# Optimization experiments

Hardware: AMD Instinct MI355X
Metric: run time of the kernel (lower is better)

The kernel has to match this reference:

```python
import jax, jax.numpy as jnp
import numpy as np

HEADS = 8
CHANNELS = 256
RR = 1
DH = CHANNELS // RR                 # per-head channels
ATT = HEADS * DH                    # 2048
# exact scale from the torch module
SCALE = (1.0 / np.sqrt(CHANNELS // RR)) / np.sqrt(2.0 / (CHANNELS + 3 * ATT)) * np.sqrt(2.0 / (CHANNELS + ATT))


def setup_inputs() -> dict:
    key = jax.random.key(0)
    k1, k2, k3, k4, k5 = jax.random.split(key, 5)
    x = jax.random.normal(k1, (8, CHANNELS, 32, 32), dtype=jnp.float32)
    # 1x1 conv weights stored as [out_ch, in_ch]
    w_in = jax.random.normal(k2, (3 * ATT, CHANNELS), dtype=jnp.float32) * (1.0 / np.sqrt(CHANNELS))
    b_in = jax.random.normal(k3, (3 * ATT,), dtype=jnp.float32) * 0.02
    w_out = jax.random.normal(k4, (CHANNELS, ATT), dtype=jnp.float32) * (1.0 / np.sqrt(ATT))
    b_out = jax.random.normal(k5, (CHANNELS,), dtype=jnp.float32) * 0.02
    return {"x": x, "w_in": w_in, "b_in": b_in, "w_out": w_out, "b_out": b_out}


def reference(x, w_in, b_in, w_out, b_out):
    n, c, h, w = x.shape
    L = h * w
    xf = x.reshape(n, c, L)
    # 1x1 conv in = channel-mixing matmul, then fixed scale
    scaled = (jnp.einsum('ncl,oc->nol', xf, w_in) + b_in[:, None]) * jnp.float32(SCALE)
    s = scaled.reshape(n, HEADS, 3 * DH, L)
    q, k, v = s[:, :, :DH], s[:, :, DH:2 * DH], s[:, :, 2 * DH:]   # each (n, H, DH, L)
    att = jnp.einsum('nhdl,nhdm->nhlm', q, k)                       # (n, H, L, L)
    # softmax over the FLATTENED L*L axis (global per head), as in the torch code
    att = jax.nn.softmax(att.reshape(n, HEADS, L * L), axis=2).reshape(n, HEADS, L, L)
    out = jnp.einsum('nhdl,nhlm->nhdm', v, att)                     # (n, H, DH, L)
    out = out.reshape(n, ATT, L)
    out = jnp.einsum('nal,ca->ncl', out, w_out) + b_out[:, None]
    return out.reshape(n, c, h, w)
```

## Files before the change

### kernel.cpp

```cpp
#include <hip/hip_runtime.h>
#include <hip/hip_bf16.h>


typedef __bf16 bf16x8 __attribute__((ext_vector_type(8)));
typedef __bf16 bf16x4 __attribute__((ext_vector_type(4)));
typedef float f32x4 __attribute__((ext_vector_type(4)));
typedef float f32x16 __attribute__((ext_vector_type(16)));
typedef __hip_bfloat16 bf16;

__device__ __forceinline__ void async_copy16(const void* g, void* s) {
    __builtin_amdgcn_global_load_lds(
        (const __attribute__((address_space(1))) unsigned int*)g,
        (__attribute__((address_space(3))) unsigned int*)s, 16, 0, 0);
}

__device__ __forceinline__ bf16x8 scale8(bf16x8 v, float s) {
    bf16x8 r;
#pragma unroll
    for (int e = 0; e < 8; ++e) r[e] = (__bf16)((float)v[e] * s);
    return r;
}

__global__ __launch_bounds__(256)
void gemm_nt(const bf16* __restrict__ A, const bf16* __restrict__ B, void* __restrict__ Cvoid,
             int M, int N, int K, int lda, int ldb, int ldc,
             long asn, long ash, long bsn, long bsh, long csn, long csh,
             int H, int mode, const float* __restrict__ bias, const float* __restrict__ Zp,
             float scale,
             bf16* __restrict__ outQ, bf16* __restrict__ outK, bf16* __restrict__ outV)
{
    __shared__ __align__(16) bf16 smem[17408];
    bf16* Alds = smem;
    bf16* Blds = smem + 8192;

    const int tid  = threadIdx.x;
    const int wave = tid >> 6;
    const int lane = tid & 63;
    const int z  = blockIdx.z;
    const int zn = z / H, zh = z % H;

    const bf16* Ab = A + zn * asn + zh * ash;
    const bf16* Bb = B + zn * bsn + zh * bsh;

    const long tM = (long)blockIdx.y * 128;
    const long tN = (long)blockIdx.x * 128;

    const int wr   = (wave >> 1) * 64;
    const int wc   = (wave & 1) * 64;
    const int l15  = lane & 15;
    const int quad = lane >> 4;

    f32x4 acc[4][4] = {};

    const int kiters = K >> 6;
    const bool regB = (mode == 4);

#pragma unroll
    for (int i = 0; i < 4; ++i) {
        const int flat = i * 256 + tid;
        const int row  = flat >> 3;
        const int kcs  = (flat & 7) ^ (row & 7);
        async_copy16(Ab + (tM + row) * (long)lda + kcs * 8,
                     (char*)Alds + (long)(i * 256 + wave * 64) * 16);
        if (!regB) {
            async_copy16(Bb + (tN + row) * (long)ldb + kcs * 8,
                         (char*)Blds + (long)(i * 256 + wave * 64) * 16);
        }
    }
    if (regB) {
        const float zi0 = 1.0f / Zp[zn * 8 + zh * 4];
#pragma unroll
        for (int i = 0; i < 4; ++i) {
            const int flat = i * 256 + tid;
            const int row  = flat >> 3;
            const int kcs  = (flat & 7) ^ (row & 7);
            bf16x8 b = *(const bf16x8*)(Bb + (tN + row) * (long)ldb + kcs * 8);
            *(bf16x8*)((char*)Blds + (long)flat * 16) = scale8(b, zi0);
        }
    }

    bf16x8 pfA[4], pfB[4];
    for (int kt = 0; kt < kiters; ++kt) {
        __syncthreads();
        const bool has_next = (kt + 1 < kiters);
        float zin = 1.0f;
        if (has_next) {
            const long kof = (long)(kt + 1) * 64;
            if (regB) zin = 1.0f / Zp[zn * 8 + zh * 4 + ((kt + 1) >> 2)];
#pragma unroll
            for (int i = 0; i < 4; ++i) {
                const int flat = i * 256 + tid;
                const int row  = flat >> 3;
                const int kcs  = (flat & 7) ^ (row & 7);
                pfA[i] = *(const bf16x8*)(Ab + (tM + row) * (long)lda + kof + kcs * 8);
                pfB[i] = *(const bf16x8*)(Bb + (tN + row) * (long)ldb + kof + kcs * 8);
            }
        }
#pragma unroll
        for (int kk = 0; kk < 2; ++kk) {
            bf16x8 af[4], bfv[4];
#pragma unroll
            for (int i = 0; i < 4; ++i) {
                const int r = wr + i * 16 + l15;
                af[i] = *(const bf16x8*)(Alds + r * 64 + ((kk * 4 + quad) ^ (r & 7)) * 8);
            }
#pragma unroll
            for (int j = 0; j < 4; ++j) {
                const int r = wc + j * 16 + l15;
                bfv[j] = *(const bf16x8*)(Blds + r * 64 + ((kk * 4 + quad) ^ (r & 7)) * 8);
            }
#pragma unroll
            for (int i = 0; i < 4; ++i)
#pragma unroll
                for (int j = 0; j < 4; ++j)
                    acc[i][j] = __builtin_amdgcn_mfma_f32_16x16x32_bf16(af[i], bfv[j], acc[i][j], 0, 0, 0);
        }
        if (has_next) {
            __builtin_amdgcn_sched_barrier(0);
            __builtin_amdgcn_s_barrier();
            __builtin_amdgcn_sched_barrier(0);
#pragma unroll
            for (int i = 0; i < 4; ++i) {
                const int flat = i * 256 + tid;
                *(bf16x8*)((char*)Alds + (long)flat * 16) = pfA[i];
                *(bf16x8*)((char*)Blds + (long)flat * 16) = regB ? scale8(pfB[i], zin) : pfB[i];
            }
        }
    }

    if (mode >= 3) {
        float* C = (float*)Cvoid + zn * csn + zh * csh;
#pragma unroll
        for (int i = 0; i < 4; ++i)
#pragma unroll
            for (int j = 0; j < 4; ++j)
#pragma unroll
                for (int r = 0; r < 4; ++r) {
                    const long row = tM + wr + i * 16 + quad * 4 + r;
                    const long col = tN + wc + j * 16 + l15;
                    if (mode == 4) {
                        const float v = acc[i][j][r] + (zh == 0 ? bias[row] : 0.0f);
                        atomicAdd(&C[row * (long)ldc + col], v);
                    } else {
                        C[row * (long)ldc + col] = acc[i][j][r] + bias[row];
                    }
                }
        return;
    }

    const int x    = blockIdx.x;
    const int part = x % 6;
    const int nh   = zn * 8 + x / 6;
    const int d0   = (part & 1) * 128;
    const int by   = blockIdx.y;

    __syncthreads();
    if (part < 4) {
#pragma unroll
        for (int i = 0; i < 4; ++i)
#pragma unroll
            for (int j = 0; j < 4; ++j)
#pragma unroll
                for (int r = 0; r < 4; ++r) {
                    const int row = wr + i * 16 + quad * 4 + r;
                    const int col = wc + j * 16 + l15;
                    const float v = (acc[i][j][r] + bias[tN + col]) * scale;
                    const int c32 = col >> 3;
                    const int slot = (c32 & 8) | ((c32 & 7) ^ (row & 7));
                    smem[row * 128 + slot * 8 + (col & 7)] = __float2bfloat16(v);
                }
        __syncthreads();
        bf16* dst = (part < 2) ? outQ : outK;
#pragma unroll
        for (int k = 0; k < 8; ++k) {
            const int flat = k * 256 + tid;
            const int seg  = flat >> 6, ln = flat & 63;
            const int lb   = seg >> 3, wloc = seg & 7;
            const int row  = lb * 32 + (ln & 31);
            const int c32  = wloc * 2 + (ln >> 5);
            const int slot = (c32 & 8) | ((c32 & 7) ^ (row & 7));
            const f32x4 val = *(const f32x4*)(smem + row * 128 + slot * 8);
            const long addr = ((long)(nh * 32 + by * 4 + lb) * 16 + (d0 >> 4) + wloc) * 512 + ln * 8;
            *(f32x4*)(dst + addr) = val;
        }
    } else {
#pragma unroll
        for (int i = 0; i < 4; ++i)
#pragma unroll
            for (int j = 0; j < 4; ++j)
#pragma unroll
                for (int r = 0; r < 4; ++r) {
                    const int row = wr + i * 16 + quad * 4 + r;
                    const int col = wc + j * 16 + l15;
                    const float v = (acc[i][j][r] + bias[tN + col]) * scale;
                    const int rc = row >> 3;
                    const int slotT = (rc & 8) | ((rc & 7) ^ (col & 7));
                    smem[col * 128 + slotT * 8 + (row & 7)] = __float2bfloat16(v);
                }
        __syncthreads();
#pragma unroll
        for (int k = 0; k < 8; ++k) {
            const int flat = k * 256 + tid;
            const int seg  = flat >> 6, ln = flat & 63;
            const int kwl  = seg >> 2, g2l = seg & 3;
            const int dl   = g2l * 32 + (ln & 31);
            const int lc   = kwl * 2 + (ln >> 5);
            const int slotT = (lc & 8) | ((lc & 7) ^ (dl & 7));
            const f32x4 val = *(const f32x4*)(smem + dl * 128 + slotT * 8);
            const long addr = ((long)(nh * 64 + by * 8 + kwl) * 8 + (d0 >> 5) + g2l) * 512 + ln * 8;
            *(f32x4*)(outV + addr) = val;
        }
    }
}

__global__ __launch_bounds__(256, 2)
void attn_fused(const bf16* __restrict__ Qsw, const bf16* __restrict__ Ksw,
                const bf16* __restrict__ Vsw, bf16* __restrict__ out_tt,
                float* __restrict__ Z)
{
    __shared__ __align__(16) bf16 smem[16904];
    bf16* Ps  = smem;
    float* Zs = (float*)(smem + 16896);

    const int tid  = threadIdx.x;
    const int wave = tid >> 6, lane = tid & 63;
    const int l31  = lane & 31, hw = lane >> 5;

    const int b   = blockIdx.x;
    const int xcd = b & 7, s = b >> 3;
    const int nh  = xcd * 8 + (s >> 4);
    const int mt  = s & 15;
    const int n   = nh >> 3, h = nh & 7;
    const long m0 = (long)mt * 64;

    const int wl = wave & 1, wm = wave >> 1;

    bf16x8 Kf[16];
    {
        const bf16* kb = Ksw + ((long)(nh * 32 + mt * 2 + wm) * 16) * 512 + lane * 8;
#pragma unroll
        for (int w = 0; w < 16; ++w)
            Kf[w] = *(const bf16x8*)(kb + w * 512);
    }
    bf16x8 Qc[16];
    {
        const bf16* qb = Qsw + ((long)(nh * 32 + wl) * 16) * 512 + lane * 8;
#pragma unroll
        for (int w = 0; w < 16; ++w)
            Qc[w] = *(const bf16x8*)(qb + w * 512);
    }

    f32x16 accO[2][2] = {};
    float zsum = 0.0f;

    for (int lt = 0; lt < 16; ++lt) {
        bf16x8 vf[4][2];
#pragma unroll
        for (int kw = 0; kw < 4; ++kw)
#pragma unroll
            for (int dt = 0; dt < 2; ++dt)
                vf[kw][dt] = *(const bf16x8*)(
                    Vsw + ((long)(nh * 64 + lt * 4 + kw) * 8 + wave * 2 + dt) * 512 + lane * 8);

        f32x16 a0 = {}, a1 = {};
#pragma unroll
        for (int w = 0; w < 16; w += 2) {
            a0 = __builtin_amdgcn_mfma_f32_32x32x16_bf16(Qc[w], Kf[w], a0, 0, 0, 0);
            a1 = __builtin_amdgcn_mfma_f32_32x32x16_bf16(Qc[w + 1], Kf[w + 1], a1, 0, 0, 0);
        }

        bf16* Pb = Ps + (lt & 1) * 6144;
#pragma unroll
        for (int g = 0; g < 4; ++g) {
            bf16x4 pk;
#pragma unroll
            for (int e = 0; e < 4; ++e) {
                const float v = __expf(a0[g * 4 + e] + a1[g * 4 + e]);
                zsum += v;
                pk[e] = (__bf16)v;
            }
            const int l  = wl * 32 + 4 * hw + 8 * g;
            const int kw = l >> 4, off = l & 15;
            *(bf16x4*)(Pb + kw * 1536 + (wm * 32 + l31) * 24 + off) = pk;
        }

        __syncthreads();

        if (lt < 15) {
            const bf16* qn = Qsw + ((long)(nh * 32 + (lt + 1) * 2 + wl) * 16) * 512 + lane * 8;
#pragma unroll
            for (int w = 0; w < 16; ++w)
                Qc[w] = *(const bf16x8*)(qn + w * 512);
        }

#pragma unroll
        for (int kw = 0; kw < 4; ++kw) {
            bf16x8 pf[2];
#pragma unroll
            for (int mh = 0; mh < 2; ++mh)
                pf[mh] = *(const bf16x8*)(Pb + kw * 1536 + (mh * 32 + l31) * 24 + hw * 8);
#pragma unroll
            for (int mh = 0; mh < 2; ++mh)
#pragma unroll
                for (int dt = 0; dt < 2; ++dt)
                    accO[mh][dt] = __builtin_amdgcn_mfma_f32_32x32x16_bf16(
                        pf[mh], vf[kw][dt], accO[mh][dt], 0, 0, 0);
        }
    }

    __syncthreads();

#pragma unroll
    for (int o = 32; o > 0; o >>= 1) zsum += __shfl_down(zsum, o);
    if (lane == 0) Zs[wave] = zsum;

    bf16* Cs = smem;
#pragma unroll
    for (int mh = 0; mh < 2; ++mh)
#pragma unroll
        for (int dt = 0; dt < 2; ++dt)
#pragma unroll
            for (int r = 0; r < 16; ++r) {
                const int m = mh * 32 + (r & 3) + 8 * (r >> 2) + 4 * hw;
                const int d = wave * 64 + dt * 32 + l31;
                Cs[m * 264 + d] = __float2bfloat16(accO[mh][dt][r]);
            }
    __syncthreads();
    if (tid == 0) atomicAdd(Z + nh, (Zs[0] + Zs[1]) + (Zs[2] + Zs[3]));

    bf16* Ob = out_tt + (long)n * 2097152 + m0 * 2048 + h * 256;
#pragma unroll
    for (int k = 0; k < 8; ++k) {
        const int flat = k * 256 + tid;
        const int row  = flat >> 5;
        const int c    = flat & 31;
        const f32x4 val = *(const f32x4*)((const char*)Cs + row * 528 + c * 16);
        *(f32x4*)((char*)(Ob + (long)row * 2048) + c * 16) = val;
    }
}

__global__ void prep_convert(const float* __restrict__ w_in, const float* __restrict__ w_out,
                             bf16* __restrict__ w_in_b, bf16* __restrict__ w_out_b,
                             float* __restrict__ Z, float* __restrict__ out)
{
    const long gid = (long)blockIdx.x * 256 + threadIdx.x;
    if (blockIdx.x == 0 && threadIdx.x < 64) Z[threadIdx.x] = 0.0f;
    const f32x4 z4 = {0.0f, 0.0f, 0.0f, 0.0f};
    if (gid < 524288) ((f32x4*)out)[gid] = z4;
    const long n1 = 6144L * 256;
    const long n2 = 256L * 2048;
    const long stride = (long)gridDim.x * 256;
    for (long i = gid; i < n1; i += stride) w_in_b[i] = __float2bfloat16(w_in[i]);
    for (long i = gid; i < n2; i += stride) w_out_b[i] = __float2bfloat16(w_out[i]);
}

__global__ void prep_xt(const float* __restrict__ x, bf16* __restrict__ x_t)
{
    __shared__ float tile[64][65];
    const int b = blockIdx.x;
    const int n = blockIdx.y;
    const int ct = b & 3, lt = b >> 2;
    const int t = threadIdx.x;
    const float* xp = x + (long)n * 256 * 1024;
#pragma unroll
    for (int i = 0; i < 16; ++i) {
        const int flat = i * 256 + t;
        const int cl = flat >> 6, ll = flat & 63;
        tile[cl][ll] = xp[(long)(ct * 64 + cl) * 1024 + lt * 64 + ll];
    }
    __syncthreads();
    bf16* xo = x_t + (long)n * 1024 * 256;
#pragma unroll
    for (int i = 0; i < 16; ++i) {
        const int flat = i * 256 + t;
        const int lr = flat >> 6, cr = flat & 63;
        xo[(long)(lt * 64 + lr) * 256 + ct * 64 + cr] = __float2bfloat16(tile[cr][lr]);
    }
}

extern "C" void kernel_launch(void* const* d_in, const int* in_sizes, int n_in,
                              void* d_out, int out_size, void* d_ws, size_t ws_size,
                              hipStream_t stream)
{
    const float* x     = (const float*)d_in[0];
    const float* w_in  = (const float*)d_in[1];
    const float* b_in  = (const float*)d_in[2];
    const float* w_out = (const float*)d_in[3];
    const float* b_out = (const float*)d_in[4];
    float* out = (float*)d_out;

    const float SCALE = 0.10416666666666667f;

    char* p = (char*)d_ws;
    bf16* Qsw     = (bf16*)p;  p += 33554432;
    bf16* Ksw     = (bf16*)p;  p += 33554432;
    bf16* Vsw     = (bf16*)p;  p += 33554432;
    bf16* out_tt  = (bf16*)p;  p += 33554432;
    bf16* x_t     = (bf16*)p;  p += 4194304;
    bf16* w_in_b  = (bf16*)p;  p += 3145728;
    bf16* w_out_b = (bf16*)p;  p += 1048576;
    float* Z      = (float*)p; p += 256;

    prep_convert<<<2048, 256, 0, stream>>>(w_in, w_out, w_in_b, w_out_b, Z, out);
    prep_xt<<<dim3(64, 8), 256, 0, stream>>>(x, x_t);

    gemm_nt<<<dim3(48, 8, 8), 256, 0, stream>>>(
        x_t, w_in_b, nullptr,
        1024, 6144, 256, 256, 256, 0,
        1024L * 256, 0, 0, 0, 0, 0,
        1, 0, b_in, nullptr, SCALE, Qsw, Ksw, Vsw);

    attn_fused<<<1024, 256, 0, stream>>>(Qsw, Ksw, Vsw, out_tt, Z);

    gemm_nt<<<dim3(8, 2, 16), 256, 0, stream>>>(
        w_out_b, out_tt, out,
        256, 1024, 1024, 2048, 2048, 1024,
        0, 1024, 1024L * 2048, 1024, 256L * 1024, 0,
        2, 4, b_out, Z, 1.0f, nullptr, nullptr, nullptr);
}
```

Baseline: 234.3 us.

## Add dedicated QKV projection kernel reading MFMA-fragment-swizzled inputs directly to registers

Replaces the generic LDS-staged GEMM for the QKV input projection with a dedicated kernel. The prep kernels now write x and w_in in a pre-swizzled layout that matches the 32x32x16 MFMA fragment order, so each lane loads its operands straight from global memory into registers through a 3-stage register pipeline, with no LDS staging or barriers in the K loop. The QKV epilogue moves into the new kernel and the generic GEMM keeps only the fp32 output path. The trade-off is no operand reuse through LDS, so every wave fetches its own fragments from global memory or L2.

```diff
diff --git a/kernel.cpp b/kernel.cpp
--- a/kernel.cpp
+++ b/kernel.cpp
@@ -22,12 +22,129 @@
 }
 
 __global__ __launch_bounds__(256)
+void proj_qkv(const bf16* __restrict__ Axw, const bf16* __restrict__ Wsw,
+              const float* __restrict__ bias, float scale,
+              bf16* __restrict__ outQ, bf16* __restrict__ outK, bf16* __restrict__ outV)
+{
+    __shared__ __align__(16) bf16 smem[16384];
+
+    const int tid  = threadIdx.x;
+    const int wave = tid >> 6, lane = tid & 63;
+    const int l31  = lane & 31, hw = lane >> 5;
+
+    const int b  = blockIdx.x;
+    const int n  = b & 7;
+    const int s  = b >> 3;
+    const int ht = s / 48;
+    const int r_ = s % 48;
+    const int part = r_ % 6;
+    const int lt   = r_ / 6;
+    const int nh = n * 8 + ht;
+    const int o0 = ht * 768 + part * 128;
+    const int d0 = (part & 1) * 128;
+
+    const int wl = wave & 1, wo = wave >> 1;
+
+    const bf16* Ap0 = Axw + ((long)(n * 32 + lt * 4 + wl * 2) * 16) * 512 + lane * 8;
+    const bf16* Ap1 = Ap0 + 16 * 512;
+    const bf16* Bp0 = Wsw + ((long)(ht * 24 + part * 4 + wo * 2) * 16) * 512 + lane * 8;
+    const bf16* Bp1 = Bp0 + 16 * 512;
+
+    bf16x8 Af[3][2], Bf[3][2];
+#pragma unroll
+    for (int p = 0; p < 3; ++p) {
+        Af[p][0] = *(const bf16x8*)(Ap0 + p * 512);
+        Af[p][1] = *(const bf16x8*)(Ap1 + p * 512);
+        Bf[p][0] = *(const bf16x8*)(Bp0 + p * 512);
+        Bf[p][1] = *(const bf16x8*)(Bp1 + p * 512);
+    }
+
+    f32x16 acc[2][2] = {};
+#pragma unroll
+    for (int k = 0; k < 16; ++k) {
+        const int st = k % 3;
+#pragma unroll
+        for (int i = 0; i < 2; ++i)
+#pragma unroll
+            for (int j = 0; j < 2; ++j)
+                acc[i][j] = __builtin_amdgcn_mfma_f32_32x32x16_bf16(
+                    Af[st][i], Bf[st][j], acc[i][j], 0, 0, 0);
+        if (k + 3 < 16) {
+            Af[st][0] = *(const bf16x8*)(Ap0 + (k + 3) * 512);
+            Af[st][1] = *(const bf16x8*)(Ap1 + (k + 3) * 512);
+            Bf[st][0] = *(const bf16x8*)(Bp0 + (k + 3) * 512);
+            Bf[st][1] = *(const bf16x8*)(Bp1 + (k + 3) * 512);
+        }
+    }
+
+    float bv[2];
+#pragma unroll
+    for (int j = 0; j < 2; ++j) bv[j] = bias[o0 + wo * 64 + j * 32 + l31];
+
+    if (part < 4) {
+#pragma unroll
+        for (int i = 0; i < 2; ++i)
+#pragma unroll
+            for (int j = 0; j < 2; ++j)
+#pragma unroll
+                for (int r = 0; r < 16; ++r) {
+                    const int row = wl * 64 + i * 32 + (r & 3) + 8 * (r >> 2) + 4 * hw;
+                    const int col = wo * 64 + j * 32 + l31;
+                    const float v = (acc[i][j][r] + bv[j]) * scale;
+                    const int c32 = col >> 3;
+                    const int slot = (c32 & 8) | ((c32 & 7) ^ (row & 7));
+                    smem[row * 128 + slot * 8 + (col & 7)] = __float2bfloat16(v);
+                }
+        __syncthreads();
+        bf16* dst = (part < 2) ? outQ : outK;
+#pragma unroll
+        for (int k = 0; k < 8; ++k) {
+            const int flat = k * 256 + tid;
+            const int seg  = flat >> 6, ln = flat & 63;
+            const int lb   = seg >> 3, wloc = seg & 7;
+            const int row  = lb * 32 + (ln & 31);
+            const int c32  = wloc * 2 + (ln >> 5);
+            const int slot = (c32 & 8) | ((c32 & 7) ^ (row & 7));
+            const f32x4 val = *(const f32x4*)(smem + row * 128 + slot * 8);
+            const long addr = ((long)(nh * 32 + lt * 4 + lb) * 16 + (d0 >> 4) + wloc) * 512 + ln * 8;
+            *(f32x4*)(dst + addr) = val;
+        }
+    } else {
+#pragma unroll
+        for (int i = 0; i < 2; ++i)
+#pragma unroll
+            for (int j = 0; j < 2; ++j)
+#pragma unroll
+                for (int r = 0; r < 16; ++r) {
+                    const int row = wl * 64 + i * 32 + (r & 3) + 8 * (r >> 2) + 4 * hw;
+                    const int col = wo * 64 + j * 32 + l31;
+                    const float v = (acc[i][j][r] + bv[j]) * scale;
+                    const int rc = row >> 3;
+                    const int slotT = (rc & 8) | ((rc & 7) ^ (col & 7));
+                    smem[col * 128 + slotT * 8 + (row & 7)] = __float2bfloat16(v);
+                }
+        __syncthreads();
+#pragma unroll
+        for (int k = 0; k < 8; ++k) {
+            const int flat = k * 256 + tid;
+            const int seg  = flat >> 6, ln = flat & 63;
+            const int kwl  = seg >> 2, g2l = seg & 3;
+            const int dl   = g2l * 32 + (ln & 31);
+            const int lc   = kwl * 2 + (ln >> 5);
+            const int slotT = (lc & 8) | ((lc & 7) ^ (dl & 7));
+            const f32x4 val = *(const f32x4*)(smem + dl * 128 + slotT * 8);
+            const long addr = ((long)(nh * 64 + lt * 8 + kwl) * 8 + (d0 >> 5) + g2l) * 512 + ln * 8;
+            *(f32x4*)(outV + addr) = val;
+        }
+    }
+}
+
+__global__ __launch_bounds__(256)
 void gemm_nt(const bf16* __restrict__ A, const bf16* __restrict__ B, void* __restrict__ Cvoid,
              int M, int N, int K, int lda, int ldb, int ldc,
              long asn, long ash, long bsn, long bsh, long csn, long csh,
              int H, int mode, const float* __restrict__ bias, const float* __restrict__ Zp,
-             float scale,
-             bf16* __restrict__ outQ, bf16* __restrict__ outK, bf16* __restrict__ outV)
+             float scale)
 {
     __shared__ __align__(16) bf16 smem[17408];
     bf16* Alds = smem;
@@ -74,8 +191,8 @@
             const int flat = i * 256 + tid;
             const int row  = flat >> 3;
             const int kcs  = (flat & 7) ^ (row & 7);
-            bf16x8 b = *(const bf16x8*)(Bb + (tN + row) * (long)ldb + kcs * 8);
-            *(bf16x8*)((char*)Blds + (long)flat * 16) = scale8(b, zi0);
+            bf16x8 bv = *(const bf16x8*)(Bb + (tN + row) * (long)ldb + kcs * 8);
+            *(bf16x8*)((char*)Blds + (long)flat * 16) = scale8(bv, zi0);
         }
     }
 
@@ -128,89 +245,22 @@
         }
     }
 
-    if (mode >= 3) {
-        float* C = (float*)Cvoid + zn * csn + zh * csh;
-#pragma unroll
-        for (int i = 0; i < 4; ++i)
-#pragma unroll
-            for (int j = 0; j < 4; ++j)
-#pragma unroll
-                for (int r = 0; r < 4; ++r) {
-                    const long row = tM + wr + i * 16 + quad * 4 + r;
-                    const long col = tN + wc + j * 16 + l15;
-                    if (mode == 4) {
-                        const float v = acc[i][j][r] + (zh == 0 ? bias[row] : 0.0f);
-                        atomicAdd(&C[row * (long)ldc + col], v);
-                    } else {
-                        C[row * (long)ldc + col] = acc[i][j][r] + bias[row];
-                    }
+    float* C = (float*)Cvoid + zn * csn + zh * csh;
+#pragma unroll
+    for (int i = 0; i < 4; ++i)
+#pragma unroll
+        for (int j = 0; j < 4; ++j)
+#pragma unroll
+            for (int r = 0; r < 4; ++r) {
+                const long row = tM + wr + i * 16 + quad * 4 + r;
+                const long col = tN + wc + j * 16 + l15;
+                if (mode == 4) {
+                    const float v = acc[i][j][r] + (zh == 0 ? bias[row] : 0.0f);
+                    atomicAdd(&C[row * (long)ldc + col], v);
+                } else {
+                    C[row * (long)ldc + col] = acc[i][j][r] + bias[row];
                 }
-        return;
-    }
-
-    const int x    = blockIdx.x;
-    const int part = x % 6;
-    const int nh   = zn * 8 + x / 6;
-    const int d0   = (part & 1) * 128;
-    const int by   = blockIdx.y;
-
-    __syncthreads();
-    if (part < 4) {
-#pragma unroll
-        for (int i = 0; i < 4; ++i)
-#pragma unroll
-            for (int j = 0; j < 4; ++j)
-#pragma unroll
-                for (int r = 0; r < 4; ++r) {
-                    const int row = wr + i * 16 + quad * 4 + r;
-                    const int col = wc + j * 16 + l15;
-                    const float v = (acc[i][j][r] + bias[tN + col]) * scale;
-                    const int c32 = col >> 3;
-                    const int slot = (c32 & 8) | ((c32 & 7) ^ (row & 7));
-                    smem[row * 128 + slot * 8 + (col & 7)] = __float2bfloat16(v);
-                }
-        __syncthreads();
-        bf16* dst = (part < 2) ? outQ : outK;
-#pragma unroll
-        for (int k = 0; k < 8; ++k) {
-            const int flat = k * 256 + tid;
-            const int seg  = flat >> 6, ln = flat & 63;
-            const int lb   = seg >> 3, wloc = seg & 7;
-            const int row  = lb * 32 + (ln & 31);
-            const int c32  = wloc * 2 + (ln >> 5);
-            const int slot = (c32 & 8) | ((c32 & 7) ^ (row & 7));
-            const f32x4 val = *(const f32x4*)(smem + row * 128 + slot * 8);
-            const long addr = ((long)(nh * 32 + by * 4 + lb) * 16 + (d0 >> 4) + wloc) * 512 + ln * 8;
-            *(f32x4*)(dst + addr) = val;
-        }
-    } else {
-#pragma unroll
-        for (int i = 0; i < 4; ++i)
-#pragma unroll
-            for (int j = 0; j < 4; ++j)
-#pragma unroll
-                for (int r = 0; r < 4; ++r) {
-                    const int row = wr + i * 16 + quad * 4 + r;
-                    const int col = wc + j * 16 + l15;
-                    const float v = (acc[i][j][r] + bias[tN + col]) * scale;
-                    const int rc = row >> 3;
-                    const int slotT = (rc & 8) | ((rc & 7) ^ (col & 7));
-                    smem[col * 128 + slotT * 8 + (row & 7)] = __float2bfloat16(v);
-                }
-        __syncthreads();
-#pragma unroll
-        for (int k = 0; k < 8; ++k) {
-            const int flat = k * 256 + tid;
-            const int seg  = flat >> 6, ln = flat & 63;
-            const int kwl  = seg >> 2, g2l = seg & 3;
-            const int dl   = g2l * 32 + (ln & 31);
-            const int lc   = kwl * 2 + (ln >> 5);
-            const int slotT = (lc & 8) | ((lc & 7) ^ (dl & 7));
-            const f32x4 val = *(const f32x4*)(smem + dl * 128 + slotT * 8);
-            const long addr = ((long)(nh * 64 + by * 8 + kwl) * 8 + (d0 >> 5) + g2l) * 512 + ln * 8;
-            *(f32x4*)(outV + addr) = val;
-        }
-    }
+            }
 }
 
 __global__ __launch_bounds__(256, 2)
@@ -340,7 +390,7 @@
 }
 
 __global__ void prep_convert(const float* __restrict__ w_in, const float* __restrict__ w_out,
-                             bf16* __restrict__ w_in_b, bf16* __restrict__ w_out_b,
+                             bf16* __restrict__ Wsw, bf16* __restrict__ w_out_b,
                              float* __restrict__ Z, float* __restrict__ out)
 {
     const long gid = (long)blockIdx.x * 256 + threadIdx.x;
@@ -350,11 +400,16 @@
     const long n1 = 6144L * 256;
     const long n2 = 256L * 2048;
     const long stride = (long)gridDim.x * 256;
-    for (long i = gid; i < n1; i += stride) w_in_b[i] = __float2bfloat16(w_in[i]);
+    for (long i = gid; i < n1; i += stride) {
+        const int o = (int)(i >> 8), c = (int)(i & 255);
+        const long addr = ((long)((o >> 5) * 16 + (c >> 4))) * 512
+                        + ((o & 31) + 32 * ((c >> 3) & 1)) * 8 + (c & 7);
+        Wsw[addr] = __float2bfloat16(w_in[i]);
+    }
     for (long i = gid; i < n2; i += stride) w_out_b[i] = __float2bfloat16(w_out[i]);
 }
 
-__global__ void prep_xt(const float* __restrict__ x, bf16* __restrict__ x_t)
+__global__ void prep_xt(const float* __restrict__ x, bf16* __restrict__ Axw)
 {
     __shared__ float tile[64][65];
     const int b = blockIdx.x;
@@ -369,12 +424,14 @@
         tile[cl][ll] = xp[(long)(ct * 64 + cl) * 1024 + lt * 64 + ll];
     }
     __syncthreads();
-    bf16* xo = x_t + (long)n * 1024 * 256;
 #pragma unroll
     for (int i = 0; i < 16; ++i) {
         const int flat = i * 256 + t;
         const int lr = flat >> 6, cr = flat & 63;
-        xo[(long)(lt * 64 + lr) * 256 + ct * 64 + cr] = __float2bfloat16(tile[cr][lr]);
+        const int l = lt * 64 + lr, c = ct * 64 + cr;
+        const long addr = ((long)((n * 32 + (l >> 5)) * 16 + (c >> 4))) * 512
+                        + ((l & 31) + 32 * ((c >> 3) & 1)) * 8 + (c & 7);
+        Axw[addr] = __float2bfloat16(tile[cr][lr]);
     }
 }
 
@@ -396,19 +453,15 @@
     bf16* Ksw     = (bf16*)p;  p += 33554432;
     bf16* Vsw     = (bf16*)p;  p += 33554432;
     bf16* out_tt  = (bf16*)p;  p += 33554432;
-    bf16* x_t     = (bf16*)p;  p += 4194304;
-    bf16* w_in_b  = (bf16*)p;  p += 3145728;
+    bf16* Axw     = (bf16*)p;  p += 4194304;
+    bf16* Wsw     = (bf16*)p;  p += 3145728;
     bf16* w_out_b = (bf16*)p;  p += 1048576;
     float* Z      = (float*)p; p += 256;
 
-    prep_convert<<<2048, 256, 0, stream>>>(w_in, w_out, w_in_b, w_out_b, Z, out);
-    prep_xt<<<dim3(64, 8), 256, 0, stream>>>(x, x_t);
-
-    gemm_nt<<<dim3(48, 8, 8), 256, 0, stream>>>(
-        x_t, w_in_b, nullptr,
-        1024, 6144, 256, 256, 256, 0,
-        1024L * 256, 0, 0, 0, 0, 0,
-        1, 0, b_in, nullptr, SCALE, Qsw, Ksw, Vsw);
+    prep_convert<<<2048, 256, 0, stream>>>(w_in, w_out, Wsw, w_out_b, Z, out);
+    prep_xt<<<dim3(64, 8), 256, 0, stream>>>(x, Axw);
+
+    proj_qkv<<<3072, 256, 0, stream>>>(Axw, Wsw, b_in, SCALE, Qsw, Ksw, Vsw);
 
     attn_fused<<<1024, 256, 0, stream>>>(Qsw, Ksw, Vsw, out_tt, Z);
 
@@ -416,5 +469,5 @@
         w_out_b, out_tt, out,
         256, 1024, 1024, 2048, 2048, 1024,
         0, 1024, 1024L * 2048, 1024, 256L * 1024, 0,
-        2, 4, b_out, Z, 1.0f, nullptr, nullptr, nullptr);
-}
+        2, 4, b_out, Z, 1.0f);
+}
```

Result: no change. 232.1 us (-0.9%).
